# Kernel optimization log

Measured on AMD Instinct MI355X. Metric: run time of the kernel, lower is better.

## Reference

```python
import jax, jax.numpy as jnp
import numpy as np

NH = 8       # num_heads
EDIM = 256   # embedding_dim (also per-head dim in this module)
BS, SQL = 4, 1024


def setup_inputs() -> dict:
    key = jax.random.key(0)
    ks = jax.random.split(key, 5)
    scale_in = 1.0 / np.sqrt(EDIM)
    scale_out = 1.0 / np.sqrt(NH * EDIM)
    return {
        "x": jax.random.normal(ks[0], (BS, SQL, EDIM), dtype=jnp.float32),
        "w_attn": jax.random.normal(ks[1], (NH * 3 * EDIM, EDIM), dtype=jnp.float32) * scale_in,
        "b_attn": jax.random.normal(ks[2], (NH * 3 * EDIM,), dtype=jnp.float32) * scale_in,
        "w_out": jax.random.normal(ks[3], (EDIM, NH * EDIM), dtype=jnp.float32) * scale_out,
        "b_out": jax.random.normal(ks[4], (EDIM,), dtype=jnp.float32) * scale_out,
    }


def reference(x, w_attn, b_attn, w_out, b_out):
    bs, sql, edim = x.shape
    nh = NH
    # projections: (bs, sql, nh*3*edim); split into Q, K, V chunks of nh*edim
    proj = x @ w_attn.T + b_attn
    q, k, v = jnp.split(proj, 3, axis=-1)
    # Faithful to torch: raw view (bs, sql, nh*edim) -> (bs, nh, sql, edim),
    # a reinterpretation of memory, NOT a transpose.
    q = q.reshape(bs, nh, sql, edim)
    k = k.reshape(bs, nh, sql, edim)
    v = v.reshape(bs, nh, sql, edim)
    # scaled dot-product scores: (bs, nh, sql, sql)
    scores = jnp.einsum("bhqd,bhkd->bhqk", q, k) / jnp.sqrt(jnp.float32(edim))
    # causal mask: -inf strictly above the diagonal (equivalent to adding triu(-inf, 1))
    causal = jnp.tril(jnp.ones((sql, sql), dtype=bool))
    scores = jnp.where(causal, scores, -jnp.inf)
    attn = jax.nn.softmax(scores, axis=-1)
    out = jnp.einsum("bhqk,bhkd->bhqd", attn, v)
    # Faithful raw view back: (bs, nh, sql, edim) -> (bs, sql, nh*edim)
    out = out.reshape(bs, sql, nh * edim)
    return out @ w_out.T + b_out
```

## Files before the change

### kernel.cpp

```cpp
#include <hip/hip_runtime.h>

#define SQL  1024
#define EDIM 256
#define NHD  8
#define NKV  (NHD * 3 * EDIM)
#define MROWS (4 * SQL)

typedef short bf16x8 __attribute__((ext_vector_type(8)));
typedef float f32x4 __attribute__((ext_vector_type(4)));

__device__ __forceinline__ unsigned short f2bf(float f) {
  unsigned u = __float_as_uint(f);
  u += 0x7fff + ((u >> 16) & 1);
  return (unsigned short)(u >> 16);
}

__device__ __forceinline__ void g2lds16(const void* g, void* l) {
  __builtin_amdgcn_global_load_lds(
      (const __attribute__((address_space(1))) unsigned int*)g,
      (__attribute__((address_space(3))) unsigned int*)l, 16, 0, 0);
}

__device__ __forceinline__ void storev(float* p, float v) { *p = v; }
__device__ __forceinline__ void storev(unsigned short* p, float v) { *p = f2bf(v); }

__global__ __launch_bounds__(256) void cast_bf16(
    const float* __restrict__ in, unsigned short* __restrict__ out, int n8) {
  int i = blockIdx.x * 256 + threadIdx.x;
  if (i >= n8) return;
  float4 a = ((const float4*)in)[2 * i];
  float4 b = ((const float4*)in)[2 * i + 1];
  union { unsigned short s[8]; ulonglong2 v; } u;
  u.s[0] = f2bf(a.x); u.s[1] = f2bf(a.y); u.s[2] = f2bf(a.z); u.s[3] = f2bf(a.w);
  u.s[4] = f2bf(b.x); u.s[5] = f2bf(b.y); u.s[6] = f2bf(b.z); u.s[7] = f2bf(b.w);
  ((ulonglong2*)out)[i] = u.v;
}

template <int BM, int BN, typename OutT>
__global__ __launch_bounds__(256) void gemm_mfma(
    const unsigned short* __restrict__ A, const unsigned short* __restrict__ B,
    const float* __restrict__ bias, OutT* __restrict__ C,
    int M, int N, int K) {
  constexpr int TM = BM / 32, TN = BN / 32;
  __shared__ __align__(16) unsigned short As[2][BM * 32];
  __shared__ __align__(16) unsigned short Bs[2][BN * 32];
  const int tid = threadIdx.x;
  const int wave = tid >> 6, lane = tid & 63;
  const int quad = lane >> 4, l16 = lane & 15;
  const int wm = (wave >> 1) * (BM / 2), wn = (wave & 1) * (BN / 2);
  const int m0 = blockIdx.x * BM, n0 = blockIdx.y * BN;
  const int sw = (l16 >> 1) & 3;

  f32x4 acc[TM][TN];
  #pragma unroll
  for (int i = 0; i < TM; i++)
    #pragma unroll
    for (int j = 0; j < TN; j++) acc[i][j] = {0.f, 0.f, 0.f, 0.f};

  auto stage = [&](int k0, int bb) {
    #pragma unroll
    for (int it = 0; it < BM / 64; it++) {
      int flat = it * 256 + tid;
      int row = flat >> 2;
      int cg = (flat & 3) ^ ((row >> 1) & 3);
      g2lds16(A + (size_t)(m0 + row) * K + k0 + cg * 8, &As[bb][flat * 8]);
    }
    #pragma unroll
    for (int it = 0; it < BN / 64; it++) {
      int flat = it * 256 + tid;
      int row = flat >> 2;
      int cg = (flat & 3) ^ ((row >> 1) & 3);
      g2lds16(B + (size_t)(n0 + row) * K + k0 + cg * 8, &Bs[bb][flat * 8]);
    }
  };

  stage(0, 0);
  __syncthreads();
  for (int k0 = 0; k0 < K; k0 += 32) {
    const int bb = (k0 >> 5) & 1;
    if (k0 + 32 < K) stage(k0 + 32, bb ^ 1);
    bf16x8 af[TM], bf[TN];
    #pragma unroll
    for (int i = 0; i < TM; i++)
      af[i] = *(const bf16x8*)&As[bb][(wm + i * 16 + l16) * 32 + (quad ^ sw) * 8];
    #pragma unroll
    for (int j = 0; j < TN; j++)
      bf[j] = *(const bf16x8*)&Bs[bb][(wn + j * 16 + l16) * 32 + (quad ^ sw) * 8];
    #pragma unroll
    for (int i = 0; i < TM; i++)
      #pragma unroll
      for (int j = 0; j < TN; j++)
        acc[i][j] = __builtin_amdgcn_mfma_f32_16x16x32_bf16(af[i], bf[j], acc[i][j], 0, 0, 0);
    __syncthreads();
  }

  #pragma unroll
  for (int i = 0; i < TM; i++) {
    #pragma unroll
    for (int r = 0; r < 4; r++) {
      int m = m0 + wm + i * 16 + quad * 4 + r;
      #pragma unroll
      for (int j = 0; j < TN; j++) {
        int n = n0 + wn + j * 16 + l16;
        storev(&C[(size_t)m * N + n], acc[i][j][r] + bias[n]);
      }
    }
  }
}

__global__ __launch_bounds__(256) void transpose_v(
    const unsigned short* __restrict__ proj, unsigned short* __restrict__ vt) {
  __shared__ unsigned short T[64][66];
  const int tid = threadIdx.x;
  const int s0 = blockIdx.x * 64, d0 = blockIdx.y * 64, bh = blockIdx.z;
  const int b = bh >> 3, h = bh & 7;
  #pragma unroll
  for (int it = 0; it < 2; it++) {
    int c = it * 256 + tid;
    int sr = c >> 3, k8 = (c & 7) * 8;
    int s = s0 + sr;
    const unsigned short* src = proj + (size_t)(b * SQL + h * 128 + (s >> 3)) * NKV
                                + 2 * 2048 + (s & 7) * 256 + d0 + k8;
    *(ulonglong2*)&T[sr][k8] = *(const ulonglong2*)src;
  }
  __syncthreads();
  #pragma unroll
  for (int it = 0; it < 2; it++) {
    int c = it * 256 + tid;
    int dr = c >> 3, s8 = (c & 7) * 8;
    unsigned short tmp[8];
    #pragma unroll
    for (int j = 0; j < 8; j++) tmp[j] = T[s8 + j][dr];
    unsigned short* dst = vt + ((size_t)bh * EDIM + d0 + dr) * SQL + s0 + s8;
    *(ulonglong2*)dst = *(ulonglong2*)tmp;
  }
}

__global__ __launch_bounds__(256, 1) void attn_mfma(
    const unsigned short* __restrict__ proj,
    const unsigned short* __restrict__ vt,
    unsigned short* __restrict__ oflat) {
  __shared__ __align__(16) unsigned short lds[74752];

  const int tid = threadIdx.x;
  const int wave = tid >> 6, lane = tid & 63;
  const int quad = lane >> 4, l16 = lane & 15;
  const int g = blockIdx.x;
  const int bh = (g & 7) * 4 + ((g >> 3) & 3);
  const int qt = g >> 5;
  const int b = bh >> 3, h = bh & 7;
  const int q0 = qt * 128;
  unsigned short* Ps = lds + 65536 + wave * 2304;

  bf16x8 aq[2][8];
  #pragma unroll
  for (int st = 0; st < 2; st++) {
    int s = q0 + wave * 32 + st * 16 + l16;
    const unsigned short* qrow =
        proj + (size_t)(b * SQL + h * 128 + (s >> 3)) * NKV + (s & 7) * 256;
    #pragma unroll
    for (int kk = 0; kk < 8; kk++)
      aq[st][kk] = *(const bf16x8*)(qrow + kk * 32 + quad * 8);
  }

  auto stage = [&](int kt, int bb) {
    unsigned short* KsB = lds + bb * 16384;
    unsigned short* VtB = lds + 32768 + bb * 16384;
    #pragma unroll
    for (int it = 0; it < 8; it++) {
      int flat = it * 256 + tid;
      int row = flat >> 5, ch = (flat & 31) ^ (row & 7);
      int s = kt * 64 + row;
      g2lds16(proj + (size_t)(b * SQL + h * 128 + (s >> 3)) * NKV + 2048
                   + (s & 7) * 256 + ch * 8,
              KsB + flat * 8);
    }
    #pragma unroll
    for (int it = 0; it < 8; it++) {
      int flat = it * 256 + tid;
      int d = flat >> 3, ch = (flat & 7) ^ (d & 7);
      g2lds16(vt + ((size_t)bh * EDIM + d) * SQL + kt * 64 + ch * 8,
              VtB + flat * 8);
    }
  };

  f32x4 o[2][16];
  #pragma unroll
  for (int st = 0; st < 2; st++)
    #pragma unroll
    for (int t = 0; t < 16; t++) o[st][t] = {0.f, 0.f, 0.f, 0.f};
  float l_r[2][4] = {};

  const int nkt = 2 * (qt + 1);
  stage(0, 0);
  __syncthreads();

  for (int kt = 0; kt < nkt; kt++) {
    const int bb = kt & 1;
    if (kt + 1 < nkt) stage(kt + 1, bb ^ 1);
    const unsigned short* KsB = lds + bb * 16384;
    const unsigned short* VtB = lds + 32768 + bb * 16384;

    f32x4 s[2][4];
    #pragma unroll
    for (int st = 0; st < 2; st++)
      #pragma unroll
      for (int c = 0; c < 4; c++) s[st][c] = {0.f, 0.f, 0.f, 0.f};
    #pragma unroll
    for (int c = 0; c < 4; c++) {
      #pragma unroll
      for (int kk = 0; kk < 8; kk++) {
        int ch = (kk * 4 + quad) ^ (l16 & 7);
        bf16x8 bk = *(const bf16x8*)&KsB[(c * 16 + l16) * 256 + ch * 8];
        s[0][c] = __builtin_amdgcn_mfma_f32_16x16x32_bf16(aq[0][kk], bk, s[0][c], 0, 0, 0);
        s[1][c] = __builtin_amdgcn_mfma_f32_16x16x32_bf16(aq[1][kk], bk, s[1][c], 0, 0, 0);
      }
    }

    #pragma unroll
    for (int st = 0; st < 2; st++) {
      #pragma unroll
      for (int c = 0; c < 4; c++) {
        int kg = kt * 64 + c * 16 + l16;
        #pragma unroll
        for (int r = 0; r < 4; r++) {
          int qg = q0 + wave * 32 + st * 16 + quad * 4 + r;
          float p = (kg <= qg) ? __expf(s[st][c][r] * 0.0625f) : 0.f;
          l_r[st][r] += p;
          Ps[(st * 16 + quad * 4 + r) * 72 + c * 16 + l16] = f2bf(p);
        }
      }
    }

    #pragma unroll
    for (int kc = 0; kc < 2; kc++) {
      bf16x8 ap0 = *(const bf16x8*)&Ps[l16 * 72 + (kc * 4 + quad) * 8];
      bf16x8 ap1 = *(const bf16x8*)&Ps[(16 + l16) * 72 + (kc * 4 + quad) * 8];
      #pragma unroll
      for (int t = 0; t < 16; t++) {
        int ch = (kc * 4 + quad) ^ (l16 & 7);
        bf16x8 bv = *(const bf16x8*)&VtB[(t * 16 + l16) * 64 + ch * 8];
        o[0][t] = __builtin_amdgcn_mfma_f32_16x16x32_bf16(ap0, bv, o[0][t], 0, 0, 0);
        o[1][t] = __builtin_amdgcn_mfma_f32_16x16x32_bf16(ap1, bv, o[1][t], 0, 0, 0);
      }
    }
    __syncthreads();
  }

  #pragma unroll
  for (int st = 0; st < 2; st++) {
    #pragma unroll
    for (int r = 0; r < 4; r++) {
      float l = l_r[st][r];
      #pragma unroll
      for (int off = 1; off < 16; off <<= 1) l += __shfl_xor(l, off);
      float inv = 1.0f / l;
      int s = q0 + wave * 32 + st * 16 + quad * 4 + r;
      unsigned short* dst =
          oflat + (size_t)(b * SQL + h * 128 + (s >> 3)) * 2048 + (s & 7) * 256;
      #pragma unroll
      for (int t = 0; t < 16; t++)
        dst[t * 16 + l16] = f2bf(o[st][t][r] * inv);
    }
  }
}

extern "C" void kernel_launch(void* const* d_in, const int* in_sizes, int n_in,
                              void* d_out, int out_size, void* d_ws, size_t ws_size,
                              hipStream_t stream) {
  const float* x      = (const float*)d_in[0];
  const float* w_attn = (const float*)d_in[1];
  const float* b_attn = (const float*)d_in[2];
  const float* w_out  = (const float*)d_in[3];
  const float* b_out  = (const float*)d_in[4];
  float* out = (float*)d_out;

  char* p = (char*)d_ws;
  unsigned short* proj = (unsigned short*)p;  p += (size_t)MROWS * NKV * 2;
  unsigned short* obf  = (unsigned short*)p;  p += (size_t)MROWS * 2048 * 2;
  unsigned short* vtb  = (unsigned short*)p;  p += (size_t)32 * EDIM * SQL * 2;
  unsigned short* xb   = (unsigned short*)p;  p += (size_t)MROWS * EDIM * 2;
  unsigned short* wb   = (unsigned short*)p;  p += (size_t)NKV * EDIM * 2;
  unsigned short* wob  = (unsigned short*)p;

  cast_bf16<<<(MROWS * EDIM / 8 + 255) / 256, 256, 0, stream>>>(x, xb, MROWS * EDIM / 8);
  cast_bf16<<<(NKV * EDIM / 8 + 255) / 256, 256, 0, stream>>>(w_attn, wb, NKV * EDIM / 8);
  cast_bf16<<<(EDIM * 2048 / 8 + 255) / 256, 256, 0, stream>>>(w_out, wob, EDIM * 2048 / 8);

  gemm_mfma<128, 128, unsigned short><<<dim3(MROWS / 128, NKV / 128), 256, 0, stream>>>(
      xb, wb, b_attn, proj, MROWS, NKV, EDIM);
  transpose_v<<<dim3(SQL / 64, EDIM / 64, 32), 256, 0, stream>>>(proj, vtb);
  attn_mfma<<<256, 256, 0, stream>>>(proj, vtb, obf);
  gemm_mfma<64, 64, float><<<dim3(MROWS / 64, EDIM / 64), 256, 0, stream>>>(
      obf, wob, b_out, out, MROWS, EDIM, NHD * EDIM);
}
```

Before: 191.7 us.

## Split attention KV range in two blocks, shrink tiles, merge cast kernels

```diff
diff --git a/kernel.cpp b/kernel.cpp
--- a/kernel.cpp
+++ b/kernel.cpp
@@ -14,6 +14,9 @@
   u += 0x7fff + ((u >> 16) & 1);
   return (unsigned short)(u >> 16);
 }
+__device__ __forceinline__ float bf2f(unsigned short s) {
+  return __uint_as_float(((unsigned)s) << 16);
+}
 
 __device__ __forceinline__ void g2lds16(const void* g, void* l) {
   __builtin_amdgcn_global_load_lds(
@@ -24,16 +27,21 @@
 __device__ __forceinline__ void storev(float* p, float v) { *p = v; }
 __device__ __forceinline__ void storev(unsigned short* p, float v) { *p = f2bf(v); }
 
-__global__ __launch_bounds__(256) void cast_bf16(
-    const float* __restrict__ in, unsigned short* __restrict__ out, int n8) {
-  int i = blockIdx.x * 256 + threadIdx.x;
-  if (i >= n8) return;
-  float4 a = ((const float4*)in)[2 * i];
-  float4 b = ((const float4*)in)[2 * i + 1];
+__global__ __launch_bounds__(256) void cast3_bf16(
+    const float* __restrict__ x, unsigned short* __restrict__ xb,
+    const float* __restrict__ wa, unsigned short* __restrict__ wb,
+    const float* __restrict__ wo, unsigned short* __restrict__ wob) {
+  const float* src; unsigned short* dst; int i;
+  int blk = blockIdx.x;
+  if (blk < 512)       { src = x;  dst = xb;  i = blk * 256 + threadIdx.x; }
+  else if (blk < 1280) { src = wa; dst = wb;  i = (blk - 512) * 256 + threadIdx.x; }
+  else                 { src = wo; dst = wob; i = (blk - 1280) * 256 + threadIdx.x; }
+  float4 a = ((const float4*)src)[2 * i];
+  float4 b = ((const float4*)src)[2 * i + 1];
   union { unsigned short s[8]; ulonglong2 v; } u;
   u.s[0] = f2bf(a.x); u.s[1] = f2bf(a.y); u.s[2] = f2bf(a.z); u.s[3] = f2bf(a.w);
   u.s[4] = f2bf(b.x); u.s[5] = f2bf(b.y); u.s[6] = f2bf(b.z); u.s[7] = f2bf(b.w);
-  ((ulonglong2*)out)[i] = u.v;
+  ((ulonglong2*)dst)[i] = u.v;
 }
 
 template <int BM, int BN, typename OutT>
@@ -136,21 +144,26 @@
   }
 }
 
-__global__ __launch_bounds__(256, 1) void attn_mfma(
+__global__ __launch_bounds__(256) void attn_mfma(
     const unsigned short* __restrict__ proj,
     const unsigned short* __restrict__ vt,
-    unsigned short* __restrict__ oflat) {
-  __shared__ __align__(16) unsigned short lds[74752];
+    unsigned short* __restrict__ opart,
+    float* __restrict__ lpart) {
+  __shared__ __align__(16) unsigned short lds[37888];
 
   const int tid = threadIdx.x;
   const int wave = tid >> 6, lane = tid & 63;
   const int quad = lane >> 4, l16 = lane & 15;
   const int g = blockIdx.x;
-  const int bh = (g & 7) * 4 + ((g >> 3) & 3);
-  const int qt = g >> 5;
+  const int bh = g & 31;
+  const int t = g >> 5;
+  const int qt = (t < 8) ? (7 - t) : (t - 8);
+  const int ks = (t < 8) ? 0 : 1;
   const int b = bh >> 3, h = bh & 7;
   const int q0 = qt * 128;
-  unsigned short* Ps = lds + 65536 + wave * 2304;
+  const int nh = 2 * (qt + 1);
+  const int kt0 = ks * nh;
+  unsigned short* Ps = lds + 32768 + wave * 1280;
 
   bf16x8 aq[2][8];
   #pragma unroll
@@ -164,22 +177,22 @@
   }
 
   auto stage = [&](int kt, int bb) {
-    unsigned short* KsB = lds + bb * 16384;
-    unsigned short* VtB = lds + 32768 + bb * 16384;
-    #pragma unroll
-    for (int it = 0; it < 8; it++) {
+    unsigned short* KsB = lds + bb * 8192;
+    unsigned short* VtB = lds + 16384 + bb * 8192;
+    #pragma unroll
+    for (int it = 0; it < 4; it++) {
       int flat = it * 256 + tid;
       int row = flat >> 5, ch = (flat & 31) ^ (row & 7);
-      int s = kt * 64 + row;
+      int s = kt * 32 + row;
       g2lds16(proj + (size_t)(b * SQL + h * 128 + (s >> 3)) * NKV + 2048
                    + (s & 7) * 256 + ch * 8,
               KsB + flat * 8);
     }
     #pragma unroll
-    for (int it = 0; it < 8; it++) {
+    for (int it = 0; it < 4; it++) {
       int flat = it * 256 + tid;
-      int d = flat >> 3, ch = (flat & 7) ^ (d & 7);
-      g2lds16(vt + ((size_t)bh * EDIM + d) * SQL + kt * 64 + ch * 8,
+      int d = flat >> 2, ch = (flat & 3) ^ ((d >> 1) & 3);
+      g2lds16(vt + ((size_t)bh * EDIM + d) * SQL + kt * 32 + ch * 8,
               VtB + flat * 8);
     }
   };
@@ -188,26 +201,26 @@
   #pragma unroll
   for (int st = 0; st < 2; st++)
     #pragma unroll
-    for (int t = 0; t < 16; t++) o[st][t] = {0.f, 0.f, 0.f, 0.f};
+    for (int tt = 0; tt < 16; tt++) o[st][tt] = {0.f, 0.f, 0.f, 0.f};
   float l_r[2][4] = {};
 
-  const int nkt = 2 * (qt + 1);
-  stage(0, 0);
+  stage(kt0, 0);
   __syncthreads();
 
-  for (int kt = 0; kt < nkt; kt++) {
-    const int bb = kt & 1;
-    if (kt + 1 < nkt) stage(kt + 1, bb ^ 1);
-    const unsigned short* KsB = lds + bb * 16384;
-    const unsigned short* VtB = lds + 32768 + bb * 16384;
-
-    f32x4 s[2][4];
+  for (int i = 0; i < nh; i++) {
+    const int kt = kt0 + i;
+    const int bb = i & 1;
+    if (i + 1 < nh) stage(kt + 1, bb ^ 1);
+    const unsigned short* KsB = lds + bb * 8192;
+    const unsigned short* VtB = lds + 16384 + bb * 8192;
+
+    f32x4 s[2][2];
     #pragma unroll
     for (int st = 0; st < 2; st++)
       #pragma unroll
-      for (int c = 0; c < 4; c++) s[st][c] = {0.f, 0.f, 0.f, 0.f};
-    #pragma unroll
-    for (int c = 0; c < 4; c++) {
+      for (int c = 0; c < 2; c++) s[st][c] = {0.f, 0.f, 0.f, 0.f};
+    #pragma unroll
+    for (int c = 0; c < 2; c++) {
       #pragma unroll
       for (int kk = 0; kk < 8; kk++) {
         int ch = (kk * 4 + quad) ^ (l16 & 7);
@@ -220,29 +233,26 @@
     #pragma unroll
     for (int st = 0; st < 2; st++) {
       #pragma unroll
-      for (int c = 0; c < 4; c++) {
-        int kg = kt * 64 + c * 16 + l16;
+      for (int c = 0; c < 2; c++) {
+        int kg = kt * 32 + c * 16 + l16;
         #pragma unroll
         for (int r = 0; r < 4; r++) {
           int qg = q0 + wave * 32 + st * 16 + quad * 4 + r;
           float p = (kg <= qg) ? __expf(s[st][c][r] * 0.0625f) : 0.f;
           l_r[st][r] += p;
-          Ps[(st * 16 + quad * 4 + r) * 72 + c * 16 + l16] = f2bf(p);
+          Ps[(st * 16 + quad * 4 + r) * 40 + c * 16 + l16] = f2bf(p);
         }
       }
     }
 
-    #pragma unroll
-    for (int kc = 0; kc < 2; kc++) {
-      bf16x8 ap0 = *(const bf16x8*)&Ps[l16 * 72 + (kc * 4 + quad) * 8];
-      bf16x8 ap1 = *(const bf16x8*)&Ps[(16 + l16) * 72 + (kc * 4 + quad) * 8];
-      #pragma unroll
-      for (int t = 0; t < 16; t++) {
-        int ch = (kc * 4 + quad) ^ (l16 & 7);
-        bf16x8 bv = *(const bf16x8*)&VtB[(t * 16 + l16) * 64 + ch * 8];
-        o[0][t] = __builtin_amdgcn_mfma_f32_16x16x32_bf16(ap0, bv, o[0][t], 0, 0, 0);
-        o[1][t] = __builtin_amdgcn_mfma_f32_16x16x32_bf16(ap1, bv, o[1][t], 0, 0, 0);
-      }
+    bf16x8 ap0 = *(const bf16x8*)&Ps[l16 * 40 + quad * 8];
+    bf16x8 ap1 = *(const bf16x8*)&Ps[(16 + l16) * 40 + quad * 8];
+    #pragma unroll
+    for (int tt = 0; tt < 16; tt++) {
+      int ch = quad ^ ((l16 >> 1) & 3);
+      bf16x8 bv = *(const bf16x8*)&VtB[(tt * 16 + l16) * 32 + ch * 8];
+      o[0][tt] = __builtin_amdgcn_mfma_f32_16x16x32_bf16(ap0, bv, o[0][tt], 0, 0, 0);
+      o[1][tt] = __builtin_amdgcn_mfma_f32_16x16x32_bf16(ap1, bv, o[1][tt], 0, 0, 0);
     }
     __syncthreads();
   }
@@ -254,15 +264,37 @@
       float l = l_r[st][r];
       #pragma unroll
       for (int off = 1; off < 16; off <<= 1) l += __shfl_xor(l, off);
-      float inv = 1.0f / l;
+      float inv = (l > 0.f) ? 1.0f / l : 0.f;
       int s = q0 + wave * 32 + st * 16 + quad * 4 + r;
-      unsigned short* dst =
-          oflat + (size_t)(b * SQL + h * 128 + (s >> 3)) * 2048 + (s & 7) * 256;
-      #pragma unroll
-      for (int t = 0; t < 16; t++)
-        dst[t * 16 + l16] = f2bf(o[st][t][r] * inv);
-    }
-  }
+      size_t rowidx = (size_t)ks * 32768 + bh * 1024 + s;
+      if (l16 == 0) lpart[rowidx] = l;
+      unsigned short* dst = opart + rowidx * 256;
+      #pragma unroll
+      for (int tt = 0; tt < 16; tt++)
+        dst[tt * 16 + l16] = f2bf(o[st][tt][r] * inv);
+    }
+  }
+}
+
+__global__ __launch_bounds__(256) void combine_split(
+    const unsigned short* __restrict__ opart, const float* __restrict__ lpart,
+    unsigned short* __restrict__ obf) {
+  int idx = blockIdx.x * 256 + threadIdx.x;
+  int row = idx >> 5;
+  int oct = idx & 31;
+  int bh = row >> 10, s = row & 1023;
+  float l1 = lpart[row], l2 = lpart[32768 + row];
+  float w = 1.0f / (l1 + l2);
+  union { unsigned short s[8]; ulonglong2 v; } u1, u2, uo;
+  u1.v = *(const ulonglong2*)(opart + (size_t)row * 256 + oct * 8);
+  u2.v = *(const ulonglong2*)(opart + (size_t)(32768 + row) * 256 + oct * 8);
+  #pragma unroll
+  for (int j = 0; j < 8; j++)
+    uo.s[j] = f2bf((bf2f(u1.s[j]) * l1 + bf2f(u2.s[j]) * l2) * w);
+  int b = bh >> 3, h = bh & 7;
+  unsigned short* dst = obf + (size_t)(b * SQL + h * 128 + (s >> 3)) * 2048
+                        + (s & 7) * 256 + oct * 8;
+  *(ulonglong2*)dst = uo.v;
 }
 
 extern "C" void kernel_launch(void* const* d_in, const int* in_sizes, int n_in,
@@ -276,21 +308,21 @@
   float* out = (float*)d_out;
 
   char* p = (char*)d_ws;
-  unsigned short* proj = (unsigned short*)p;  p += (size_t)MROWS * NKV * 2;
-  unsigned short* obf  = (unsigned short*)p;  p += (size_t)MROWS * 2048 * 2;
-  unsigned short* vtb  = (unsigned short*)p;  p += (size_t)32 * EDIM * SQL * 2;
-  unsigned short* xb   = (unsigned short*)p;  p += (size_t)MROWS * EDIM * 2;
-  unsigned short* wb   = (unsigned short*)p;  p += (size_t)NKV * EDIM * 2;
-  unsigned short* wob  = (unsigned short*)p;
-
-  cast_bf16<<<(MROWS * EDIM / 8 + 255) / 256, 256, 0, stream>>>(x, xb, MROWS * EDIM / 8);
-  cast_bf16<<<(NKV * EDIM / 8 + 255) / 256, 256, 0, stream>>>(w_attn, wb, NKV * EDIM / 8);
-  cast_bf16<<<(EDIM * 2048 / 8 + 255) / 256, 256, 0, stream>>>(w_out, wob, EDIM * 2048 / 8);
-
+  unsigned short* proj  = (unsigned short*)p;  p += (size_t)MROWS * NKV * 2;
+  unsigned short* obf   = (unsigned short*)p;  p += (size_t)MROWS * 2048 * 2;
+  unsigned short* vtb   = (unsigned short*)p;  p += (size_t)32 * EDIM * SQL * 2;
+  unsigned short* xb    = (unsigned short*)p;  p += (size_t)MROWS * EDIM * 2;
+  unsigned short* wb    = (unsigned short*)p;  p += (size_t)NKV * EDIM * 2;
+  unsigned short* wob   = (unsigned short*)p;  p += (size_t)EDIM * 2048 * 2;
+  unsigned short* opart = (unsigned short*)p;  p += (size_t)2 * 32768 * 256 * 2;
+  float*          lpart = (float*)p;
+
+  cast3_bf16<<<1536, 256, 0, stream>>>(x, xb, w_attn, wb, w_out, wob);
   gemm_mfma<128, 128, unsigned short><<<dim3(MROWS / 128, NKV / 128), 256, 0, stream>>>(
       xb, wb, b_attn, proj, MROWS, NKV, EDIM);
   transpose_v<<<dim3(SQL / 64, EDIM / 64, 32), 256, 0, stream>>>(proj, vtb);
-  attn_mfma<<<256, 256, 0, stream>>>(proj, vtb, obf);
+  attn_mfma<<<512, 256, 0, stream>>>(proj, vtb, opart, lpart);
+  combine_split<<<4096, 256, 0, stream>>>(opart, lpart, obf);
   gemm_mfma<64, 64, float><<<dim3(MROWS / 64, EDIM / 64), 256, 0, stream>>>(
       obf, wob, b_out, out, MROWS, EDIM, NHD * EDIM);
 }
```

Result: no change. 195.2 us (+1.8%).
